# Performance work log

Measured on AMD Instinct MI355X. Metric: run time of the kernel, lower is better.

The kernel has to match this reference:

```python
import jax, jax.numpy as jnp
import numpy as np

HEADS = 20          # SDXL 1280-dim blocks use 20 heads (head_dim=64)
GROUND_SCALE = 1.0  # self.scale in the module


def _mha(q, k, v):
    # q: [B,S,C], k/v: [B,L,C] -> out [B,S,C]; diffusers get_attention_scores math
    B, S, C = q.shape
    d = C // HEADS
    qh = q.reshape(B, S, HEADS, d)
    kh = k.reshape(B, k.shape[1], HEADS, d)
    vh = v.reshape(B, v.shape[1], HEADS, d)
    scores = jnp.einsum('bqhd,bkhd->bhqk', qh, kh) * (d ** -0.5)
    probs = jax.nn.softmax(scores, axis=-1)
    out = jnp.einsum('bhqk,bkhd->bqhd', probs, vh)
    return out.reshape(B, S, C)


def setup_inputs() -> dict:
    key = jax.random.key(0)
    ks = jax.random.split(key, 13)
    B, S, C = 4, 4096, 1280      # batch, latent tokens (64x64), hidden_size
    L, Dc = 77, 2048             # text context len, cross_attention_dim
    Dt = 768                     # text grounding dim
    Ntext, Nimg = 10, 40         # num_object*num_tokens_{text,image}
    s = 0.02
    return {
        'hidden_states': jax.random.normal(ks[0], (B, S, C), jnp.float32),
        'encoder_hidden_states': jax.random.normal(ks[1], (B, L, Dc), jnp.float32),
        'text_box_grounding_embeds': jax.random.normal(ks[2], (B, Ntext, Dt), jnp.float32),
        'image_box_grounding_embeds': jax.random.normal(ks[3], (B, Nimg, Dc), jnp.float32),
        'Wq': jax.random.normal(ks[4], (C, C), jnp.float32) * s,
        'Wk': jax.random.normal(ks[5], (Dc, C), jnp.float32) * s,
        'Wv': jax.random.normal(ks[6], (Dc, C), jnp.float32) * s,
        'Wk_text': jax.random.normal(ks[7], (Dt, C), jnp.float32) * s,
        'Wv_text': jax.random.normal(ks[8], (Dt, C), jnp.float32) * s,
        'Wk_image': jax.random.normal(ks[9], (Dc, C), jnp.float32) * s,
        'Wv_image': jax.random.normal(ks[10], (Dc, C), jnp.float32) * s,
        'Wo': jax.random.normal(ks[11], (C, C), jnp.float32) * s,
        'bo': jnp.zeros((C,), jnp.float32),
    }


def reference(hidden_states, encoder_hidden_states, text_box_grounding_embeds,
              image_box_grounding_embeds, Wq, Wk, Wv, Wk_text, Wv_text,
              Wk_image, Wv_image, Wo, bo):
    residual = hidden_states
    # projections
    q = hidden_states @ Wq                       # [B,S,C]
    k = encoder_hidden_states @ Wk               # [B,L,C]
    v = encoder_hidden_states @ Wv
    # text-grounding KV appended to the text context KV
    k_text = text_box_grounding_embeds @ Wk_text # [B,Ntext,C]
    v_text = text_box_grounding_embeds @ Wv_text
    k = jnp.concatenate([k, k_text], axis=1)
    v = jnp.concatenate([v, v_text], axis=1)
    hs = _mha(q, k, v)
    # stage-2 image-grounding branch: separate attention, residual blend
    k_img = image_box_grounding_embeds @ Wk_image  # [B,Nimg,C]
    v_img = image_box_grounding_embeds @ Wv_image
    hs_img = _mha(q, k_img, v_img)
    hs = hs + GROUND_SCALE * hs_img
    # output projection (to_out[0]); dropout (to_out[1]) is identity at eval
    hs = hs @ Wo + bo
    # residual_connection=True, rescale_output_factor=1.0
    return hs + residual
```

## Files before the change

kernel.cpp:

```cpp
#include <hip/hip_runtime.h>

typedef unsigned short u16;
typedef __attribute__((ext_vector_type(4)))  float  f32x4;
typedef __attribute__((ext_vector_type(8)))  short  s16x8;
typedef __attribute__((ext_vector_type(8)))  unsigned short u16x8;
typedef __attribute__((ext_vector_type(4)))  unsigned short u16x4;
typedef __attribute__((ext_vector_type(4)))  float  f4;

#define AS1(p) ((const __attribute__((address_space(1))) void*)(p))
#define AS3(p) ((__attribute__((address_space(3))) void*)(p))

__device__ __forceinline__ float bf2f(u16 u) {
    unsigned v = ((unsigned)u) << 16;
    return __builtin_bit_cast(float, v);
}
__device__ __forceinline__ u16 f2bf(float f) {
    unsigned u = __builtin_bit_cast(unsigned, f);
    unsigned r = u + 0x7FFFu + ((u >> 16) & 1u);
    return (u16)(r >> 16);
}

struct CastJobs { const float* in[4]; u16* out[4]; long b[3]; };
__global__ void cast4_kernel(CastJobs J, long total4) {
    long i = (long)blockIdx.x * blockDim.x + threadIdx.x;
    if (i >= total4) return;
    int j = (i >= J.b[0]) + (i >= J.b[1]) + (i >= J.b[2]);
    long k = i - (j ? J.b[j - 1] : 0);
    f4 v = ((const f4*)J.in[j])[k];
    u16x4 o;
    o[0] = f2bf(v.x); o[1] = f2bf(v.y); o[2] = f2bf(v.z); o[3] = f2bf(v.w);
    ((u16x4*)J.out[j])[k] = o;
}

struct TJobs { const float* in[8]; u16* out[8]; int K[8]; };
__global__ void transpose8_kernel(TJobs J) {
    const int N = 1280;
    const int j = blockIdx.z;
    const int K = J.K[j];
    const int kb = blockIdx.y * 32;
    if (kb >= K) return;
    const float* in = J.in[j];
    u16* out = J.out[j];
    __shared__ float tile[32][33];
    int nb = blockIdx.x * 32;
    int tx = threadIdx.x, ty = threadIdx.y;
#pragma unroll
    for (int r = 0; r < 32; r += 8)
        tile[ty + r][tx] = in[(size_t)(kb + ty + r) * N + nb + tx];
    __syncthreads();
#pragma unroll
    for (int r = 0; r < 32; r += 8)
        out[(size_t)(nb + ty + r) * K + kb + tx] = f2bf(tile[tx][ty + r]);
}

#define SB __builtin_amdgcn_sched_barrier(0)
#define GATE0 do { asm volatile("s_waitcnt vmcnt(0)" ::: "memory"); SB; } while (0)

template <int EPI>
__global__ __launch_bounds__(256, 2) void gemm_8p(
    const u16* __restrict__ A, const u16* __restrict__ Bt, void* __restrict__ outp,
    const float* __restrict__ bias, const u16* __restrict__ resid)
{
    const int K = 1280, N = 1280;
    __shared__ u16 lsA[2][128 * 64];
    __shared__ u16 lsB[2][160 * 64];

    const int bid = blockIdx.x;
    const int swz = (bid & 7) * 128 + (bid >> 3);
    const int m0 = (swz >> 3) * 128;
    const int n0 = (swz & 7) * 160;

    const int t = threadIdx.x;
    const int lane = t & 63, wid = t >> 6;
    const int wm = wid >> 1, wn = wid & 1;
    const int fr = lane & 15, hi = lane >> 4;
    const int fr7 = fr & 7;

    const int srow = t >> 3;
    const int sslot = (t & 7) ^ (srow & 7);
    const u16* gA = A  + (size_t)(m0 + srow) * K + sslot * 8;
    const u16* gB = Bt + (size_t)(n0 + srow) * K + sslot * 8;
    const size_t cK = (size_t)32 * K;

#define STGA(BUF, CC, KO) __builtin_amdgcn_global_load_lds(AS1(gA + (CC) * cK + (KO)), \
        AS3((char*)lsA + (BUF) * 16384 + (CC) * 4096 + t * 16), 16, 0, 0)
#define STGB(BUF, CC, KO) __builtin_amdgcn_global_load_lds(AS1(gB + (CC) * cK + (KO)), \
        AS3((char*)lsB + (BUF) * 20480 + (CC) * 4096 + t * 16), 16, 0, 0)

#define STG9(BUF, KO) do { \
    STGB(BUF, 0, KO); STGB(BUF, 1, KO); STGB(BUF, 2, KO); STGB(BUF, 3, KO); STGB(BUF, 4, KO); \
    STGA(BUF, 0, KO); STGA(BUF, 1, KO); STGA(BUF, 2, KO); STGA(BUF, 3, KO); \
} while (0)

    const char* lA0 = (const char*)lsA + (size_t)(wm * 64 + fr) * 128 + (((0 + hi) ^ fr7) << 4);
    const char* lA1 = (const char*)lsA + (size_t)(wm * 64 + fr) * 128 + (((4 + hi) ^ fr7) << 4);
    const char* lB0 = (const char*)lsB + (size_t)(wn * 80 + fr) * 128 + (((0 + hi) ^ fr7) << 4);
    const char* lB1 = (const char*)lsB + (size_t)(wn * 80 + fr) * 128 + (((4 + hi) ^ fr7) << 4);

    f32x4 acc[4][5];
#pragma unroll
    for (int i = 0; i < 4; i++)
#pragma unroll
        for (int j = 0; j < 5; j++)
            acc[i][j] = (f32x4){0.f, 0.f, 0.f, 0.f};

    s16x8 af[4], bfv[5];

#define DSRD2(BUF, KS) do { \
    _Pragma("unroll") for (int mi = 0; mi < 4; mi++) \
        af[mi] = *(const s16x8*)(((KS) ? lA1 : lA0) + (BUF) * 16384 + mi * 2048); \
    _Pragma("unroll") for (int nf = 0; nf < 5; nf++) \
        bfv[nf] = *(const s16x8*)(((KS) ? lB1 : lB0) + (BUF) * 20480 + nf * 2048); \
} while (0)

#define MM2 do { \
    _Pragma("unroll") for (int mi = 0; mi < 4; mi++) \
        _Pragma("unroll") for (int nf = 0; nf < 5; nf++) \
            acc[mi][nf] = __builtin_amdgcn_mfma_f32_16x16x32_bf16( \
                af[mi], bfv[nf], acc[mi][nf], 0, 0, 0); \
} while (0)

#define PHA(BUF, DOSTG, KO) do { \
    DSRD2(BUF, 0); \
    if (DOSTG) STG9((BUF) ^ 1, KO); \
    SB; \
    __builtin_amdgcn_s_barrier(); \
    SB; \
    asm volatile("s_waitcnt lgkmcnt(0)" ::: "memory"); \
    SB; \
    __builtin_amdgcn_s_setprio(1); \
    MM2; \
    __builtin_amdgcn_s_setprio(0); \
    SB; \
    __builtin_amdgcn_s_barrier(); \
    SB; \
} while (0)

#define PHB(BUF, DOGATE) do { \
    DSRD2(BUF, 1); \
    SB; \
    __builtin_amdgcn_s_barrier(); \
    SB; \
    asm volatile("s_waitcnt lgkmcnt(0)" ::: "memory"); \
    SB; \
    __builtin_amdgcn_s_setprio(1); \
    MM2; \
    __builtin_amdgcn_s_setprio(0); \
    SB; \
    if (DOGATE) { GATE0; } \
    __builtin_amdgcn_s_barrier(); \
    SB; \
} while (0)

    STG9(0, 0);
    GATE0;
    __builtin_amdgcn_s_barrier();
    SB;

    for (int i = 0; i < 9; i++) {
        const size_t k1 = (size_t)(2 * i + 1) * 64, k2 = k1 + 64;
        PHA(0, 1, k1); PHB(0, 1);
        PHA(1, 1, k2); PHB(1, 1);
    }
    PHA(0, 1, (size_t)19 * 64); PHB(0, 1);
    PHA(1, 0, 0);               PHB(1, 0);

#pragma unroll
    for (int mf = 0; mf < 4; mf++) {
#pragma unroll
        for (int nf = 0; nf < 5; nf++) {
#pragma unroll
            for (int j = 0; j < 4; j++) {
                int row = m0 + wm * 64 + mf * 16 + hi * 4 + j;
                int col = n0 + wn * 80 + nf * 16 + fr;
                float v = acc[mf][nf][j];
                if constexpr (EPI == 0) {
                    ((u16*)outp)[(size_t)row * N + col] = f2bf(v);
                } else {
                    ((float*)outp)[(size_t)row * N + col] =
                        v + bias[col] + bf2f(resid[(size_t)row * N + col]);
                }
            }
        }
    }
#undef STGA
#undef STGB
#undef STG9
#undef DSRD2
#undef MM2
#undef PHA
#undef PHB
}

struct KVJobs { const u16* A[6]; const u16* Bt[6]; float* out[6]; int M[6]; int K[6]; int gx[6]; };
__global__ __launch_bounds__(256) void gemm_kv(KVJobs J) {
    const int j = blockIdx.z;
    if ((int)blockIdx.x >= J.gx[j]) return;
    const u16* A  = J.A[j];
    const u16* Bt = J.Bt[j];
    float* outp   = J.out[j];
    const int M = J.M[j], K = J.K[j], N = 1280;

    __shared__ u16 lsA[2][128 * 64];
    __shared__ u16 lsB[2][128 * 64];

    const int m0 = blockIdx.x * 128, n0 = blockIdx.y * 128;
    const int t = threadIdx.x;
    const int lane = t & 63;
    const int wid = t >> 6;
    const int wr = wid >> 1, wc = wid & 1;
    const int fr = lane & 15;
    const int fq = lane >> 4;
    const int fr7 = fr & 7;

    f32x4 acc[4][4];
#pragma unroll
    for (int i = 0; i < 4; i++)
#pragma unroll
        for (int jj = 0; jj < 4; jj++)
            acc[i][jj] = (f32x4){0.f, 0.f, 0.f, 0.f};

    const int arow = t >> 3;
    const int aslot = (t & 7) ^ (arow & 7);
    const u16* gA = A  + (size_t)(m0 + arow) * K + aslot * 8;
    const u16* gB = Bt + (size_t)(n0 + arow) * K + aslot * 8;
    const size_t cK = (size_t)32 * K;

#define STAGE(buf, k0) do { \
    _Pragma("unroll") for (int c = 0; c < 4; c++) { \
        __builtin_amdgcn_global_load_lds(AS1(gA + c * cK + (k0)), AS3((char*)lsA + (buf) * 16384 + c * 4096 + t * 16), 16, 0, 0); \
        __builtin_amdgcn_global_load_lds(AS1(gB + c * cK + (k0)), AS3((char*)lsB + (buf) * 16384 + c * 4096 + t * 16), 16, 0, 0); \
    } \
} while (0)

    const char* lA0 = (const char*)lsA + (size_t)(wr * 64 + fr) * 128 + (((0 + fq) ^ fr7) << 4);
    const char* lA1 = (const char*)lsA + (size_t)(wr * 64 + fr) * 128 + (((4 + fq) ^ fr7) << 4);
    const char* lB0 = (const char*)lsB + (size_t)(wc * 64 + fr) * 128 + (((0 + fq) ^ fr7) << 4);
    const char* lB1 = (const char*)lsB + (size_t)(wc * 64 + fr) * 128 + (((4 + fq) ^ fr7) << 4);

    STAGE(0, 0);
    __syncthreads();

    int cur = 0;
    for (int k0 = 0; k0 < K; k0 += 64) {
        if (k0 + 64 < K) STAGE(cur ^ 1, k0 + 64);

#pragma unroll
        for (int ks = 0; ks < 2; ks++) {
            s16x8 af[4], bfr[4];
#pragma unroll
            for (int i = 0; i < 4; i++) {
                af[i]  = *(const s16x8*)((ks ? lA1 : lA0) + cur * 16384 + i * 2048);
                bfr[i] = *(const s16x8*)((ks ? lB1 : lB0) + cur * 16384 + i * 2048);
            }
#pragma unroll
            for (int mi = 0; mi < 4; mi++)
#pragma unroll
                for (int ni = 0; ni < 4; ni++)
                    acc[mi][ni] = __builtin_amdgcn_mfma_f32_16x16x32_bf16(af[mi], bfr[ni], acc[mi][ni], 0, 0, 0);
        }

        __syncthreads();
        cur ^= 1;
    }
#undef STAGE

#pragma unroll
    for (int mi = 0; mi < 4; mi++) {
#pragma unroll
        for (int ni = 0; ni < 4; ni++) {
#pragma unroll
            for (int jj = 0; jj < 4; jj++) {
                int row = m0 + wr * 64 + mi * 16 + fq * 4 + jj;
                int col = n0 + wc * 64 + ni * 16 + fr;
                if (row < M)
                    outp[(size_t)row * N + col] = acc[mi][ni][jj];
            }
        }
    }
}

__global__ void gather_kv(
    const float* __restrict__ k77, const float* __restrict__ v77,
    const float* __restrict__ ktx, const float* __restrict__ vtx,
    const float* __restrict__ kim, const float* __restrict__ vim,
    u16* __restrict__ Kimg, u16* __restrict__ Vimg)
{
    const int bh = blockIdx.x;
    const int b = bh / 20, h = bh - b * 20;
    const int t = threadIdx.x;
    char* Kd = (char*)(Kimg + (size_t)bh * 8192);
    char* Vd = (char*)(Vimg + (size_t)bh * 8192);

#pragma unroll
    for (int i = 0; i < 4; i++) {
        int ch = t + i * 256;
        int r = ch >> 3, cs = ch & 7;
        u16x8 ov = (u16x8){0,0,0,0,0,0,0,0};
        if (r < 127) {
            const float* src = r < 77 ? k77 + ((size_t)b * 77 + r) * 1280
                            : r < 87  ? ktx + ((size_t)b * 10 + (r - 77)) * 1280
                                      : kim + ((size_t)b * 40 + (r - 87)) * 1280;
            const f4* s4 = (const f4*)(src + h * 64 + cs * 8);
            f4 a = s4[0], c = s4[1];
            ov[0]=f2bf(a.x*0.125f); ov[1]=f2bf(a.y*0.125f); ov[2]=f2bf(a.z*0.125f); ov[3]=f2bf(a.w*0.125f);
            ov[4]=f2bf(c.x*0.125f); ov[5]=f2bf(c.y*0.125f); ov[6]=f2bf(c.z*0.125f); ov[7]=f2bf(c.w*0.125f);
        }
        *(u16x8*)(Kd + ((r * 128 + cs * 16) ^ ((r & 7) << 4))) = ov;
    }

#pragma unroll
    for (int i = 0; i < 4; i++) {
        int ch = t + i * 256;
        int d = ch & 63, ks = ch >> 6;
        u16x8 ov;
#pragma unroll
        for (int j = 0; j < 8; j++) {
            int key = ks * 8 + j;
            float val = key < 77  ? v77[((size_t)b * 77 + key) * 1280 + h * 64 + d]
                      : key < 87  ? vtx[((size_t)b * 10 + key - 77) * 1280 + h * 64 + d]
                      : key < 127 ? vim[((size_t)b * 40 + key - 87) * 1280 + h * 64 + d]
                                  : 0.f;
            ov[j] = f2bf(val);
        }
        *(u16x8*)(Vd + ((d * 256 + ks * 16) ^ ((d & 7) << 4))) = ov;
    }
}

__global__ __launch_bounds__(256) void attn_mfma(
    const u16* __restrict__ q, const u16* __restrict__ Kimg,
    const u16* __restrict__ Vimg, u16* __restrict__ out)
{
    __shared__ char sm[49152];
    char* Qb = sm;
    char* Kb = sm + 16384;
    char* Vb = sm + 32768;

    const int t = threadIdx.x;
    const int lane = t & 63, wid = t >> 6;
    const int lo = lane & 15, hi = lane >> 4;
    const int s0 = blockIdx.x * 128;
    const int bh = blockIdx.y;
    const int b = bh / 20, h = bh - b * 20;
    const size_t rs0 = (size_t)b * 4096 + s0;

    const u16* gk = Kimg + (size_t)bh * 8192;
    const u16* gv = Vimg + (size_t)bh * 8192;
#pragma unroll
    for (int i = 0; i < 4; i++) {
        int ch = t + i * 256;
        __builtin_amdgcn_global_load_lds(AS1(gk + (size_t)ch * 8), AS3(Kb + ch * 16), 16, 0, 0);
        __builtin_amdgcn_global_load_lds(AS1(gv + (size_t)ch * 8), AS3(Vb + ch * 16), 16, 0, 0);
    }
#pragma unroll
    for (int i = 0; i < 4; i++) {
        int ch = t + i * 256;
        int r = ch >> 3, cs = ch & 7;
        u16x8 v = *(const u16x8*)(q + (rs0 + r) * 1280 + h * 64 + cs * 8);
        *(u16x8*)(Qb + ((r * 128 + cs * 16) ^ ((r & 7) << 4))) = v;
    }
    __syncthreads();

    const int m0r = wid * 32;
    s16x8 qf[2][2];
#pragma unroll
    for (int m = 0; m < 2; m++)
#pragma unroll
        for (int kf = 0; kf < 2; kf++) {
            int r = m0r + m * 16 + lo;
            qf[m][kf] = *(const s16x8*)(Qb + ((r * 128 + (kf * 4 + hi) * 16) ^ ((r & 7) << 4)));
        }
    f32x4 sc[2][8];
#pragma unroll
    for (int m = 0; m < 2; m++)
#pragma unroll
        for (int n = 0; n < 8; n++)
            sc[m][n] = (f32x4){0.f, 0.f, 0.f, 0.f};
#pragma unroll
    for (int kf = 0; kf < 2; kf++)
#pragma unroll
        for (int n = 0; n < 8; n++) {
            int r = n * 16 + lo;
            s16x8 kf8 = *(const s16x8*)(Kb + ((r * 128 + (kf * 4 + hi) * 16) ^ ((r & 7) << 4)));
#pragma unroll
            for (int m = 0; m < 2; m++)
                sc[m][n] = __builtin_amdgcn_mfma_f32_16x16x32_bf16(qf[m][kf], kf8, sc[m][n], 0, 0, 0);
        }
    __syncthreads();

    char* Pb = sm + wid * 8192;
#pragma unroll
    for (int m = 0; m < 2; m++) {
#pragma unroll
        for (int j = 0; j < 4; j++) {
            float e[8];
            float s1 = 0.f, s2 = 0.f;
#pragma unroll
            for (int n = 0; n < 8; n++) {
                int col = n * 16 + lo;
                float ev = __expf(sc[m][n][j]);
                e[n] = ev;
                if (col < 87) s1 += ev;
                else if (col < 127) s2 += ev;
            }
#pragma unroll
            for (int d = 1; d < 16; d <<= 1) {
                s1 += __shfl_xor(s1, d);
                s2 += __shfl_xor(s2, d);
            }
            float i1 = 1.f / s1, i2 = 1.f / s2;
            int row = m * 16 + hi * 4 + j;
#pragma unroll
            for (int n = 0; n < 8; n++) {
                int col = n * 16 + lo;
                float w = col < 87 ? i1 : (col < 127 ? i2 : 0.f);
                *(u16*)(Pb + ((row * 256 + col * 2) ^ ((row & 7) << 4))) = f2bf(e[n] * w);
            }
        }
    }
    __syncthreads();

    f32x4 o2[2][4];
#pragma unroll
    for (int m = 0; m < 2; m++)
#pragma unroll
        for (int n = 0; n < 4; n++)
            o2[m][n] = (f32x4){0.f, 0.f, 0.f, 0.f};
#pragma unroll
    for (int kk = 0; kk < 4; kk++) {
        s16x8 pa[2];
#pragma unroll
        for (int m = 0; m < 2; m++) {
            int row = m * 16 + lo;
            pa[m] = *(const s16x8*)(Pb + ((row * 256 + (kk * 4 + hi) * 16) ^ ((row & 7) << 4)));
        }
#pragma unroll
        for (int n = 0; n < 4; n++) {
            int dr = n * 16 + lo;
            s16x8 vf = *(const s16x8*)(Vb + ((dr * 256 + (kk * 4 + hi) * 16) ^ ((dr & 7) << 4)));
#pragma unroll
            for (int m = 0; m < 2; m++)
                o2[m][n] = __builtin_amdgcn_mfma_f32_16x16x32_bf16(pa[m], vf, o2[m][n], 0, 0, 0);
        }
    }

#pragma unroll
    for (int m = 0; m < 2; m++)
#pragma unroll
        for (int n = 0; n < 4; n++)
#pragma unroll
            for (int j = 0; j < 4; j++) {
                size_t row = rs0 + m0r + m * 16 + hi * 4 + j;
                out[row * 1280 + h * 64 + n * 16 + lo] = f2bf(o2[m][n][j]);
            }
}

extern "C" void kernel_launch(void* const* d_in, const int* in_sizes, int n_in,
                              void* d_out, int out_size, void* d_ws, size_t ws_size,
                              hipStream_t stream)
{
    const float* hs  = (const float*)d_in[0];
    const float* ehs = (const float*)d_in[1];
    const float* tbg = (const float*)d_in[2];
    const float* ibg = (const float*)d_in[3];
    const float* Wq  = (const float*)d_in[4];
    const float* Wk  = (const float*)d_in[5];
    const float* Wv  = (const float*)d_in[6];
    const float* Wkt = (const float*)d_in[7];
    const float* Wvt = (const float*)d_in[8];
    const float* Wki = (const float*)d_in[9];
    const float* Wvi = (const float*)d_in[10];
    const float* Wo  = (const float*)d_in[11];
    const float* bo  = (const float*)d_in[12];
    float* out = (float*)d_out;

    const int B = 4, S = 4096, C = 1280, L = 77, Nt = 10, Ni = 40, Dc = 2048, Dt = 768;
    const int M = B * S;

    char* p = (char*)d_ws;
    auto alloc = [&](size_t bytes) -> void* {
        void* r = (void*)p;
        p += (bytes + 255) & ~(size_t)255;
        return r;
    };
    u16* hs_b  = (u16*)alloc((size_t)M * C * 2);
    u16* q_b   = (u16*)alloc((size_t)M * C * 2);
    u16* at_b  = (u16*)alloc((size_t)M * C * 2);
    u16* WqT   = (u16*)alloc((size_t)C * C * 2);
    u16* WoT   = (u16*)alloc((size_t)C * C * 2);
    u16* WkT   = (u16*)alloc((size_t)C * Dc * 2);
    u16* WvT   = (u16*)alloc((size_t)C * Dc * 2);
    u16* WkiT  = (u16*)alloc((size_t)C * Dc * 2);
    u16* WviT  = (u16*)alloc((size_t)C * Dc * 2);
    u16* WktT  = (u16*)alloc((size_t)C * Dt * 2);
    u16* WvtT  = (u16*)alloc((size_t)C * Dt * 2);
    u16* ehs_b = (u16*)alloc((size_t)384 * Dc * 2);
    u16* tbg_b = (u16*)alloc((size_t)128 * Dt * 2);
    u16* ibg_b = (u16*)alloc((size_t)256 * Dc * 2);
    float* k77 = (float*)alloc((size_t)B * L  * C * 4);
    float* v77 = (float*)alloc((size_t)B * L  * C * 4);
    float* ktx = (float*)alloc((size_t)B * Nt * C * 4);
    float* vtx = (float*)alloc((size_t)B * Nt * C * 4);
    float* kim = (float*)alloc((size_t)B * Ni * C * 4);
    float* vim = (float*)alloc((size_t)B * Ni * C * 4);
    u16* Kimg  = (u16*)alloc((size_t)80 * 8192 * 2);
    u16* Vimg  = (u16*)alloc((size_t)80 * 8192 * 2);

    CastJobs cj;
    cj.in[0] = hs;  cj.out[0] = hs_b;
    cj.in[1] = ehs; cj.out[1] = ehs_b;
    cj.in[2] = tbg; cj.out[2] = tbg_b;
    cj.in[3] = ibg; cj.out[3] = ibg_b;
    long c0 = (long)M * C / 4, c1 = (long)B * L * Dc / 4,
         c2 = (long)B * Nt * Dt / 4, c3 = (long)B * Ni * Dc / 4;
    cj.b[0] = c0; cj.b[1] = c0 + c1; cj.b[2] = c0 + c1 + c2;
    long total4 = c0 + c1 + c2 + c3;
    cast4_kernel<<<(int)((total4 + 255) / 256), 256, 0, stream>>>(cj, total4);

    TJobs tj;
    const float* wins[8] = {Wq, Wk, Wv, Wkt, Wvt, Wki, Wvi, Wo};
    u16* wouts[8]        = {WqT, WkT, WvT, WktT, WvtT, WkiT, WviT, WoT};
    int wks[8]           = {C, Dc, Dc, Dt, Dt, Dc, Dc, C};
    for (int i = 0; i < 8; i++) { tj.in[i] = wins[i]; tj.out[i] = wouts[i]; tj.K[i] = wks[i]; }
    transpose8_kernel<<<dim3(C / 32, Dc / 32, 8), dim3(32, 8), 0, stream>>>(tj);

    gemm_8p<0><<<1024, 256, 0, stream>>>(hs_b, WqT, q_b, nullptr, nullptr);

    KVJobs kj;
    const u16* kas[6]  = {ehs_b, ehs_b, tbg_b, tbg_b, ibg_b, ibg_b};
    const u16* kbs[6]  = {WkT, WvT, WktT, WvtT, WkiT, WviT};
    float* kos[6]      = {k77, v77, ktx, vtx, kim, vim};
    int kms[6]         = {B * L, B * L, B * Nt, B * Nt, B * Ni, B * Ni};
    int kks[6]         = {Dc, Dc, Dt, Dt, Dc, Dc};
    int kgx[6]         = {3, 3, 1, 1, 2, 2};
    for (int i = 0; i < 6; i++) {
        kj.A[i] = kas[i]; kj.Bt[i] = kbs[i]; kj.out[i] = kos[i];
        kj.M[i] = kms[i]; kj.K[i] = kks[i]; kj.gx[i] = kgx[i];
    }
    gemm_kv<<<dim3(3, C / 128, 6), 256, 0, stream>>>(kj);

    gather_kv<<<80, 256, 0, stream>>>(k77, v77, ktx, vtx, kim, vim, Kimg, Vimg);
    attn_mfma<<<dim3(S / 128, B * 20), 256, 0, stream>>>(q_b, Kimg, Vimg, at_b);

    gemm_8p<2><<<1024, 256, 0, stream>>>(at_b, WoT, out, bo, hs_b);
}
```

Baseline: 252.6 us.

## Merge prep kernels, fuse Q and KV GEMMs, write attention K/V layout directly

Merges the cast and weight-transpose kernels into one launch. Runs the Q-projection GEMM and all six KV-projection GEMMs as one grid, with the KV blocks scheduled first. The KV blocks now write scaled bf16 results straight into the swizzled per-head K/V layouts that attention expects, replacing the fp32 intermediates and the separate gather kernel. This removes several launches and an fp32 round trip through memory, at the cost of a memset for padding and scattered 2-byte stores in the KV epilogue.

```diff
diff --git a/kernel.cpp b/kernel.cpp
--- a/kernel.cpp
+++ b/kernel.cpp
@@ -20,41 +20,46 @@
     return (u16)(r >> 16);
 }
 
-struct CastJobs { const float* in[4]; u16* out[4]; long b[3]; };
-__global__ void cast4_kernel(CastJobs J, long total4) {
-    long i = (long)blockIdx.x * blockDim.x + threadIdx.x;
-    if (i >= total4) return;
-    int j = (i >= J.b[0]) + (i >= J.b[1]) + (i >= J.b[2]);
-    long k = i - (j ? J.b[j - 1] : 0);
-    f4 v = ((const f4*)J.in[j])[k];
-    u16x4 o;
-    o[0] = f2bf(v.x); o[1] = f2bf(v.y); o[2] = f2bf(v.z); o[3] = f2bf(v.w);
-    ((u16x4*)J.out[j])[k] = o;
-}
-
-struct TJobs { const float* in[8]; u16* out[8]; int K[8]; };
-__global__ void transpose8_kernel(TJobs J) {
-    const int N = 1280;
-    const int j = blockIdx.z;
-    const int K = J.K[j];
-    const int kb = blockIdx.y * 32;
-    if (kb >= K) return;
-    const float* in = J.in[j];
-    u16* out = J.out[j];
+#define SB __builtin_amdgcn_sched_barrier(0)
+#define GATE0 do { asm volatile("s_waitcnt vmcnt(0)" ::: "memory"); SB; } while (0)
+
+struct PrepJobs {
+    const float* cin[4]; u16* cout[4]; long cb[3];
+    const float* tin[8]; u16* tout[8]; int tK[8];
+};
+__global__ __launch_bounds__(256) void prep_kernel(PrepJobs J) {
+    const int bid = blockIdx.x;
+    const int t = threadIdx.x;
+    if (bid < 21446) {
+        long i = (long)bid * 256 + t;
+        int j = (i >= J.cb[0]) + (i >= J.cb[1]) + (i >= J.cb[2]);
+        long k = i - (j ? J.cb[j - 1] : 0);
+        f4 v = ((const f4*)J.cin[j])[k];
+        u16x4 o;
+        o[0] = f2bf(v.x); o[1] = f2bf(v.y); o[2] = f2bf(v.z); o[3] = f2bf(v.w);
+        ((u16x4*)J.cout[j])[k] = o;
+        return;
+    }
+    int u = bid - 21446;
+    int j = (u >= 1600) + (u >= 4160) + (u >= 6720) + (u >= 7680)
+          + (u >= 8640) + (u >= 11200) + (u >= 13760);
+    const int cumprev[8] = {0, 1600, 4160, 6720, 7680, 8640, 11200, 13760};
+    int rem = u - cumprev[j];
+    const float* in = J.tin[j];
+    u16* out = J.tout[j];
+    const int K = J.tK[j];
+    const int nb = (rem % 40) * 32;
+    const int kb = (rem / 40) * 32;
     __shared__ float tile[32][33];
-    int nb = blockIdx.x * 32;
-    int tx = threadIdx.x, ty = threadIdx.y;
+    const int tx = t & 31, ty = t >> 5;
 #pragma unroll
     for (int r = 0; r < 32; r += 8)
-        tile[ty + r][tx] = in[(size_t)(kb + ty + r) * N + nb + tx];
+        tile[ty + r][tx] = in[(size_t)(kb + ty + r) * 1280 + nb + tx];
     __syncthreads();
 #pragma unroll
     for (int r = 0; r < 32; r += 8)
         out[(size_t)(nb + ty + r) * K + kb + tx] = f2bf(tile[tx][ty + r]);
 }
-
-#define SB __builtin_amdgcn_sched_barrier(0)
-#define GATE0 do { asm volatile("s_waitcnt vmcnt(0)" ::: "memory"); SB; } while (0)
 
 template <int EPI>
 __global__ __launch_bounds__(256, 2) void gemm_8p(
@@ -86,7 +91,6 @@
         AS3((char*)lsA + (BUF) * 16384 + (CC) * 4096 + t * 16), 16, 0, 0)
 #define STGB(BUF, CC, KO) __builtin_amdgcn_global_load_lds(AS1(gB + (CC) * cK + (KO)), \
         AS3((char*)lsB + (BUF) * 20480 + (CC) * 4096 + t * 16), 16, 0, 0)
-
 #define STG9(BUF, KO) do { \
     STGB(BUF, 0, KO); STGB(BUF, 1, KO); STGB(BUF, 2, KO); STGB(BUF, 3, KO); STGB(BUF, 4, KO); \
     STGA(BUF, 0, KO); STGA(BUF, 1, KO); STGA(BUF, 2, KO); STGA(BUF, 3, KO); \
@@ -112,44 +116,27 @@
     _Pragma("unroll") for (int nf = 0; nf < 5; nf++) \
         bfv[nf] = *(const s16x8*)(((KS) ? lB1 : lB0) + (BUF) * 20480 + nf * 2048); \
 } while (0)
-
 #define MM2 do { \
     _Pragma("unroll") for (int mi = 0; mi < 4; mi++) \
         _Pragma("unroll") for (int nf = 0; nf < 5; nf++) \
             acc[mi][nf] = __builtin_amdgcn_mfma_f32_16x16x32_bf16( \
                 af[mi], bfv[nf], acc[mi][nf], 0, 0, 0); \
 } while (0)
-
 #define PHA(BUF, DOSTG, KO) do { \
     DSRD2(BUF, 0); \
     if (DOSTG) STG9((BUF) ^ 1, KO); \
-    SB; \
-    __builtin_amdgcn_s_barrier(); \
-    SB; \
-    asm volatile("s_waitcnt lgkmcnt(0)" ::: "memory"); \
-    SB; \
-    __builtin_amdgcn_s_setprio(1); \
-    MM2; \
-    __builtin_amdgcn_s_setprio(0); \
-    SB; \
-    __builtin_amdgcn_s_barrier(); \
-    SB; \
-} while (0)
-
+    SB; __builtin_amdgcn_s_barrier(); SB; \
+    asm volatile("s_waitcnt lgkmcnt(0)" ::: "memory"); SB; \
+    __builtin_amdgcn_s_setprio(1); MM2; __builtin_amdgcn_s_setprio(0); SB; \
+    __builtin_amdgcn_s_barrier(); SB; \
+} while (0)
 #define PHB(BUF, DOGATE) do { \
     DSRD2(BUF, 1); \
-    SB; \
-    __builtin_amdgcn_s_barrier(); \
-    SB; \
-    asm volatile("s_waitcnt lgkmcnt(0)" ::: "memory"); \
-    SB; \
-    __builtin_amdgcn_s_setprio(1); \
-    MM2; \
-    __builtin_amdgcn_s_setprio(0); \
-    SB; \
+    SB; __builtin_amdgcn_s_barrier(); SB; \
+    asm volatile("s_waitcnt lgkmcnt(0)" ::: "memory"); SB; \
+    __builtin_amdgcn_s_setprio(1); MM2; __builtin_amdgcn_s_setprio(0); SB; \
     if (DOGATE) { GATE0; } \
-    __builtin_amdgcn_s_barrier(); \
-    SB; \
+    __builtin_amdgcn_s_barrier(); SB; \
 } while (0)
 
     STG9(0, 0);
@@ -192,26 +179,134 @@
 #undef PHB
 }
 
-struct KVJobs { const u16* A[6]; const u16* Bt[6]; float* out[6]; int M[6]; int K[6]; int gx[6]; };
-__global__ __launch_bounds__(256) void gemm_kv(KVJobs J) {
-    const int j = blockIdx.z;
-    if ((int)blockIdx.x >= J.gx[j]) return;
+struct FKV {
+    const u16* A[6]; const u16* Bt[6];
+    int K[6], M[6], L[6], base[6];
+    u16 *Kimg, *Vimg;
+};
+__global__ __launch_bounds__(256, 2) void gemm_fused(
+    const u16* __restrict__ Aq, const u16* __restrict__ Bq, u16* __restrict__ outq, FKV J)
+{
+    __shared__ char smem[73728];
+    const int t = threadIdx.x;
+    const int lane = t & 63, wid = t >> 6;
+    const int fr = lane & 15, hi = lane >> 4;
+    const int fr7 = fr & 7;
+
+    if (blockIdx.x >= 120) {
+        const int K = 1280, N = 1280;
+        const int bid = blockIdx.x - 120;
+        const int swz = (bid & 7) * 128 + (bid >> 3);
+        const int m0 = (swz >> 3) * 128;
+        const int n0 = (swz & 7) * 160;
+        const int wm = wid >> 1, wn = wid & 1;
+        const int srow = t >> 3;
+        const int sslot = (t & 7) ^ (srow & 7);
+        const u16* gA = Aq + (size_t)(m0 + srow) * K + sslot * 8;
+        const u16* gB = Bq + (size_t)(n0 + srow) * K + sslot * 8;
+        const size_t cK = (size_t)32 * K;
+
+#define QSTGA(BUF, CC, KO) __builtin_amdgcn_global_load_lds(AS1(gA + (CC) * cK + (KO)), \
+        AS3(smem + (BUF) * 16384 + (CC) * 4096 + t * 16), 16, 0, 0)
+#define QSTGB(BUF, CC, KO) __builtin_amdgcn_global_load_lds(AS1(gB + (CC) * cK + (KO)), \
+        AS3(smem + 32768 + (BUF) * 20480 + (CC) * 4096 + t * 16), 16, 0, 0)
+#define QSTG9(BUF, KO) do { \
+    QSTGB(BUF, 0, KO); QSTGB(BUF, 1, KO); QSTGB(BUF, 2, KO); QSTGB(BUF, 3, KO); QSTGB(BUF, 4, KO); \
+    QSTGA(BUF, 0, KO); QSTGA(BUF, 1, KO); QSTGA(BUF, 2, KO); QSTGA(BUF, 3, KO); \
+} while (0)
+
+        const char* lA0 = smem + (size_t)(wm * 64 + fr) * 128 + (((0 + hi) ^ fr7) << 4);
+        const char* lA1 = smem + (size_t)(wm * 64 + fr) * 128 + (((4 + hi) ^ fr7) << 4);
+        const char* lB0 = smem + 32768 + (size_t)(wn * 80 + fr) * 128 + (((0 + hi) ^ fr7) << 4);
+        const char* lB1 = smem + 32768 + (size_t)(wn * 80 + fr) * 128 + (((4 + hi) ^ fr7) << 4);
+
+        f32x4 acc[4][5];
+#pragma unroll
+        for (int i = 0; i < 4; i++)
+#pragma unroll
+            for (int j = 0; j < 5; j++)
+                acc[i][j] = (f32x4){0.f, 0.f, 0.f, 0.f};
+
+        s16x8 af[4], bfv[5];
+
+#define QDSRD2(BUF, KS) do { \
+    _Pragma("unroll") for (int mi = 0; mi < 4; mi++) \
+        af[mi] = *(const s16x8*)(((KS) ? lA1 : lA0) + (BUF) * 16384 + mi * 2048); \
+    _Pragma("unroll") for (int nf = 0; nf < 5; nf++) \
+        bfv[nf] = *(const s16x8*)(((KS) ? lB1 : lB0) + (BUF) * 20480 + nf * 2048); \
+} while (0)
+#define QMM2 do { \
+    _Pragma("unroll") for (int mi = 0; mi < 4; mi++) \
+        _Pragma("unroll") for (int nf = 0; nf < 5; nf++) \
+            acc[mi][nf] = __builtin_amdgcn_mfma_f32_16x16x32_bf16( \
+                af[mi], bfv[nf], acc[mi][nf], 0, 0, 0); \
+} while (0)
+#define QPHA(BUF, DOSTG, KO) do { \
+    QDSRD2(BUF, 0); \
+    if (DOSTG) QSTG9((BUF) ^ 1, KO); \
+    SB; __builtin_amdgcn_s_barrier(); SB; \
+    asm volatile("s_waitcnt lgkmcnt(0)" ::: "memory"); SB; \
+    __builtin_amdgcn_s_setprio(1); QMM2; __builtin_amdgcn_s_setprio(0); SB; \
+    __builtin_amdgcn_s_barrier(); SB; \
+} while (0)
+#define QPHB(BUF, DOGATE) do { \
+    QDSRD2(BUF, 1); \
+    SB; __builtin_amdgcn_s_barrier(); SB; \
+    asm volatile("s_waitcnt lgkmcnt(0)" ::: "memory"); SB; \
+    __builtin_amdgcn_s_setprio(1); QMM2; __builtin_amdgcn_s_setprio(0); SB; \
+    if (DOGATE) { GATE0; } \
+    __builtin_amdgcn_s_barrier(); SB; \
+} while (0)
+
+        QSTG9(0, 0);
+        GATE0;
+        __builtin_amdgcn_s_barrier();
+        SB;
+
+        for (int i = 0; i < 9; i++) {
+            const size_t k1 = (size_t)(2 * i + 1) * 64, k2 = k1 + 64;
+            QPHA(0, 1, k1); QPHB(0, 1);
+            QPHA(1, 1, k2); QPHB(1, 1);
+        }
+        QPHA(0, 1, (size_t)19 * 64); QPHB(0, 1);
+        QPHA(1, 0, 0);               QPHB(1, 0);
+
+#pragma unroll
+        for (int mf = 0; mf < 4; mf++) {
+#pragma unroll
+            for (int nf = 0; nf < 5; nf++) {
+#pragma unroll
+                for (int j = 0; j < 4; j++) {
+                    int row = m0 + wm * 64 + mf * 16 + hi * 4 + j;
+                    int col = n0 + wn * 80 + nf * 16 + fr;
+                    outq[(size_t)row * 1280 + col] = f2bf(acc[mf][nf][j]);
+                }
+            }
+        }
+#undef QSTGA
+#undef QSTGB
+#undef QSTG9
+#undef QDSRD2
+#undef QMM2
+#undef QPHA
+#undef QPHB
+        return;
+    }
+
+    const int kvq = blockIdx.x;
+    const int pn = kvq % 10;
+    const int rem = kvq / 10;
+    int j, bx;
+    if (rem < 6)      { j = rem / 3;            bx = rem % 3; }
+    else if (rem < 8) { j = rem - 4;            bx = 0; }
+    else              { j = 4 + ((rem - 8) >> 1); bx = (rem - 8) & 1; }
+
     const u16* A  = J.A[j];
     const u16* Bt = J.Bt[j];
-    float* outp   = J.out[j];
-    const int M = J.M[j], K = J.K[j], N = 1280;
-
-    __shared__ u16 lsA[2][128 * 64];
-    __shared__ u16 lsB[2][128 * 64];
-
-    const int m0 = blockIdx.x * 128, n0 = blockIdx.y * 128;
-    const int t = threadIdx.x;
-    const int lane = t & 63;
-    const int wid = t >> 6;
+    const int K = J.K[j], Mj = J.M[j], Lj = J.L[j], basej = J.base[j];
+    const int m0 = bx * 128, n0 = pn * 128;
     const int wr = wid >> 1, wc = wid & 1;
-    const int fr = lane & 15;
-    const int fq = lane >> 4;
-    const int fr7 = fr & 7;
+    const int fq = hi;
 
     f32x4 acc[4][4];
 #pragma unroll
@@ -226,24 +321,24 @@
     const u16* gB = Bt + (size_t)(n0 + arow) * K + aslot * 8;
     const size_t cK = (size_t)32 * K;
 
-#define STAGE(buf, k0) do { \
+#define KSTAGE(buf, k0) do { \
     _Pragma("unroll") for (int c = 0; c < 4; c++) { \
-        __builtin_amdgcn_global_load_lds(AS1(gA + c * cK + (k0)), AS3((char*)lsA + (buf) * 16384 + c * 4096 + t * 16), 16, 0, 0); \
-        __builtin_amdgcn_global_load_lds(AS1(gB + c * cK + (k0)), AS3((char*)lsB + (buf) * 16384 + c * 4096 + t * 16), 16, 0, 0); \
+        __builtin_amdgcn_global_load_lds(AS1(gA + c * cK + (k0)), AS3(smem + (buf) * 16384 + c * 4096 + t * 16), 16, 0, 0); \
+        __builtin_amdgcn_global_load_lds(AS1(gB + c * cK + (k0)), AS3(smem + 32768 + (buf) * 16384 + c * 4096 + t * 16), 16, 0, 0); \
     } \
 } while (0)
 
-    const char* lA0 = (const char*)lsA + (size_t)(wr * 64 + fr) * 128 + (((0 + fq) ^ fr7) << 4);
-    const char* lA1 = (const char*)lsA + (size_t)(wr * 64 + fr) * 128 + (((4 + fq) ^ fr7) << 4);
-    const char* lB0 = (const char*)lsB + (size_t)(wc * 64 + fr) * 128 + (((0 + fq) ^ fr7) << 4);
-    const char* lB1 = (const char*)lsB + (size_t)(wc * 64 + fr) * 128 + (((4 + fq) ^ fr7) << 4);
-
-    STAGE(0, 0);
+    const char* lA0 = smem + (size_t)(wr * 64 + fr) * 128 + (((0 + fq) ^ fr7) << 4);
+    const char* lA1 = smem + (size_t)(wr * 64 + fr) * 128 + (((4 + fq) ^ fr7) << 4);
+    const char* lB0 = smem + 32768 + (size_t)(wc * 64 + fr) * 128 + (((0 + fq) ^ fr7) << 4);
+    const char* lB1 = smem + 32768 + (size_t)(wc * 64 + fr) * 128 + (((4 + fq) ^ fr7) << 4);
+
+    KSTAGE(0, 0);
     __syncthreads();
 
     int cur = 0;
     for (int k0 = 0; k0 < K; k0 += 64) {
-        if (k0 + 64 < K) STAGE(cur ^ 1, k0 + 64);
+        if (k0 + 64 < K) KSTAGE(cur ^ 1, k0 + 64);
 
 #pragma unroll
         for (int ks = 0; ks < 2; ks++) {
@@ -263,8 +358,11 @@
         __syncthreads();
         cur ^= 1;
     }
-#undef STAGE
-
+#undef KSTAGE
+
+    const bool isV = (j & 1) != 0;
+    u16* img = isV ? J.Vimg : J.Kimg;
+    const float scl = isV ? 1.0f : 0.125f;
 #pragma unroll
     for (int mi = 0; mi < 4; mi++) {
 #pragma unroll
@@ -272,58 +370,17 @@
 #pragma unroll
             for (int jj = 0; jj < 4; jj++) {
                 int row = m0 + wr * 64 + mi * 16 + fq * 4 + jj;
-                int col = n0 + wc * 64 + ni * 16 + fr;
-                if (row < M)
-                    outp[(size_t)row * N + col] = acc[mi][ni][jj];
-            }
-        }
-    }
-}
-
-__global__ void gather_kv(
-    const float* __restrict__ k77, const float* __restrict__ v77,
-    const float* __restrict__ ktx, const float* __restrict__ vtx,
-    const float* __restrict__ kim, const float* __restrict__ vim,
-    u16* __restrict__ Kimg, u16* __restrict__ Vimg)
-{
-    const int bh = blockIdx.x;
-    const int b = bh / 20, h = bh - b * 20;
-    const int t = threadIdx.x;
-    char* Kd = (char*)(Kimg + (size_t)bh * 8192);
-    char* Vd = (char*)(Vimg + (size_t)bh * 8192);
-
-#pragma unroll
-    for (int i = 0; i < 4; i++) {
-        int ch = t + i * 256;
-        int r = ch >> 3, cs = ch & 7;
-        u16x8 ov = (u16x8){0,0,0,0,0,0,0,0};
-        if (r < 127) {
-            const float* src = r < 77 ? k77 + ((size_t)b * 77 + r) * 1280
-                            : r < 87  ? ktx + ((size_t)b * 10 + (r - 77)) * 1280
-                                      : kim + ((size_t)b * 40 + (r - 87)) * 1280;
-            const f4* s4 = (const f4*)(src + h * 64 + cs * 8);
-            f4 a = s4[0], c = s4[1];
-            ov[0]=f2bf(a.x*0.125f); ov[1]=f2bf(a.y*0.125f); ov[2]=f2bf(a.z*0.125f); ov[3]=f2bf(a.w*0.125f);
-            ov[4]=f2bf(c.x*0.125f); ov[5]=f2bf(c.y*0.125f); ov[6]=f2bf(c.z*0.125f); ov[7]=f2bf(c.w*0.125f);
-        }
-        *(u16x8*)(Kd + ((r * 128 + cs * 16) ^ ((r & 7) << 4))) = ov;
-    }
-
-#pragma unroll
-    for (int i = 0; i < 4; i++) {
-        int ch = t + i * 256;
-        int d = ch & 63, ks = ch >> 6;
-        u16x8 ov;
-#pragma unroll
-        for (int j = 0; j < 8; j++) {
-            int key = ks * 8 + j;
-            float val = key < 77  ? v77[((size_t)b * 77 + key) * 1280 + h * 64 + d]
-                      : key < 87  ? vtx[((size_t)b * 10 + key - 77) * 1280 + h * 64 + d]
-                      : key < 127 ? vim[((size_t)b * 40 + key - 87) * 1280 + h * 64 + d]
-                                  : 0.f;
-            ov[j] = f2bf(val);
-        }
-        *(u16x8*)(Vd + ((d * 256 + ks * 16) ^ ((d & 7) << 4))) = ov;
+                if (row < Mj) {
+                    int col = n0 + wc * 64 + ni * 16 + fr;
+                    int b = row / Lj, kl = row - b * Lj, kg = basej + kl;
+                    int h = col >> 6, d = col & 63;
+                    size_t bhoff = (size_t)(b * 20 + h) * 16384;
+                    int off = isV ? (((d * 256 + (kg >> 3) * 16) ^ ((d & 7) << 4)) + (kg & 7) * 2)
+                                  : (((kg * 128 + (d >> 3) * 16) ^ ((kg & 7) << 4)) + (d & 7) * 2);
+                    *(u16*)((char*)img + bhoff + off) = f2bf(acc[mi][ni][jj] * scl);
+                }
+            }
+        }
     }
 }
 
@@ -497,49 +554,39 @@
     u16* ehs_b = (u16*)alloc((size_t)384 * Dc * 2);
     u16* tbg_b = (u16*)alloc((size_t)128 * Dt * 2);
     u16* ibg_b = (u16*)alloc((size_t)256 * Dc * 2);
-    float* k77 = (float*)alloc((size_t)B * L  * C * 4);
-    float* v77 = (float*)alloc((size_t)B * L  * C * 4);
-    float* ktx = (float*)alloc((size_t)B * Nt * C * 4);
-    float* vtx = (float*)alloc((size_t)B * Nt * C * 4);
-    float* kim = (float*)alloc((size_t)B * Ni * C * 4);
-    float* vim = (float*)alloc((size_t)B * Ni * C * 4);
     u16* Kimg  = (u16*)alloc((size_t)80 * 8192 * 2);
     u16* Vimg  = (u16*)alloc((size_t)80 * 8192 * 2);
 
-    CastJobs cj;
-    cj.in[0] = hs;  cj.out[0] = hs_b;
-    cj.in[1] = ehs; cj.out[1] = ehs_b;
-    cj.in[2] = tbg; cj.out[2] = tbg_b;
-    cj.in[3] = ibg; cj.out[3] = ibg_b;
+    hipMemsetAsync(Kimg, 0, (size_t)2 * 80 * 8192 * 2, stream);
+
+    PrepJobs pj;
+    pj.cin[0] = hs;  pj.cout[0] = hs_b;
+    pj.cin[1] = ehs; pj.cout[1] = ehs_b;
+    pj.cin[2] = tbg; pj.cout[2] = tbg_b;
+    pj.cin[3] = ibg; pj.cout[3] = ibg_b;
     long c0 = (long)M * C / 4, c1 = (long)B * L * Dc / 4,
          c2 = (long)B * Nt * Dt / 4, c3 = (long)B * Ni * Dc / 4;
-    cj.b[0] = c0; cj.b[1] = c0 + c1; cj.b[2] = c0 + c1 + c2;
-    long total4 = c0 + c1 + c2 + c3;
-    cast4_kernel<<<(int)((total4 + 255) / 256), 256, 0, stream>>>(cj, total4);
-
-    TJobs tj;
+    pj.cb[0] = c0; pj.cb[1] = c0 + c1; pj.cb[2] = c0 + c1 + c2;
     const float* wins[8] = {Wq, Wk, Wv, Wkt, Wvt, Wki, Wvi, Wo};
     u16* wouts[8]        = {WqT, WkT, WvT, WktT, WvtT, WkiT, WviT, WoT};
     int wks[8]           = {C, Dc, Dc, Dt, Dt, Dc, Dc, C};
-    for (int i = 0; i < 8; i++) { tj.in[i] = wins[i]; tj.out[i] = wouts[i]; tj.K[i] = wks[i]; }
-    transpose8_kernel<<<dim3(C / 32, Dc / 32, 8), dim3(32, 8), 0, stream>>>(tj);
-
-    gemm_8p<0><<<1024, 256, 0, stream>>>(hs_b, WqT, q_b, nullptr, nullptr);
-
-    KVJobs kj;
+    for (int i = 0; i < 8; i++) { pj.tin[i] = wins[i]; pj.tout[i] = wouts[i]; pj.tK[i] = wks[i]; }
+    prep_kernel<<<21446 + 15360, 256, 0, stream>>>(pj);
+
+    FKV fk;
     const u16* kas[6]  = {ehs_b, ehs_b, tbg_b, tbg_b, ibg_b, ibg_b};
     const u16* kbs[6]  = {WkT, WvT, WktT, WvtT, WkiT, WviT};
-    float* kos[6]      = {k77, v77, ktx, vtx, kim, vim};
-    int kms[6]         = {B * L, B * L, B * Nt, B * Nt, B * Ni, B * Ni};
-    int kks[6]         = {Dc, Dc, Dt, Dt, Dc, Dc};
-    int kgx[6]         = {3, 3, 1, 1, 2, 2};
+    int kks[6]   = {Dc, Dc, Dt, Dt, Dc, Dc};
+    int kms[6]   = {B * L, B * L, B * Nt, B * Nt, B * Ni, B * Ni};
+    int kls[6]   = {L, L, Nt, Nt, Ni, Ni};
+    int kbase[6] = {0, 0, 77, 77, 87, 87};
     for (int i = 0; i < 6; i++) {
-        kj.A[i] = kas[i]; kj.Bt[i] = kbs[i]; kj.out[i] = kos[i];
-        kj.M[i] = kms[i]; kj.K[i] = kks[i]; kj.gx[i] = kgx[i];
-    }
-    gemm_kv<<<dim3(3, C / 128, 6), 256, 0, stream>>>(kj);
-
-    gather_kv<<<80, 256, 0, stream>>>(k77, v77, ktx, vtx, kim, vim, Kimg, Vimg);
+        fk.A[i] = kas[i]; fk.Bt[i] = kbs[i];
+        fk.K[i] = kks[i]; fk.M[i] = kms[i]; fk.L[i] = kls[i]; fk.base[i] = kbase[i];
+    }
+    fk.Kimg = Kimg; fk.Vimg = Vimg;
+    gemm_fused<<<120 + 1024, 256, 0, stream>>>(hs_b, WqT, q_b, fk);
+
     attn_mfma<<<dim3(S / 128, B * 20), 256, 0, stream>>>(q_b, Kimg, Vimg, at_b);
 
     gemm_8p<2><<<1024, 256, 0, stream>>>(at_b, WoT, out, bo, hs_b);
```

New measurement: 220.2 us. -12.8%, faster.
